# Optimization experiments

Measured on AMD Instinct MI355X. Metric: run time of the kernel, lower is better.

## Reference

```python
import jax, jax.numpy as jnp
import numpy as np
from jax import lax

M_BLOCKS = 4
D = 768
N = 8
L = 2040  # divisible by 1,2,3,4 so every block is full, matching the floor-based slicing


def setup_inputs() -> dict:
    key = jax.random.key(0)
    ks = jax.random.split(key, 7)
    X = jax.random.normal(ks[0], (N, L, D), dtype=jnp.float32)
    # char_mixer: Conv1d(d, d, kernel_size=3, padding='same')
    conv_w = jax.random.normal(ks[1], (D, D, 3), dtype=jnp.float32) * (1.0 / np.sqrt(3 * D))
    conv_b = jax.random.normal(ks[2], (D,), dtype=jnp.float32) * 0.01
    # F_R: Linear(d, 1)
    wr = jax.random.normal(ks[3], (D, 1), dtype=jnp.float32) * (1.0 / np.sqrt(D))
    br = jax.random.normal(ks[4], (1,), dtype=jnp.float32) * 0.01
    # F_D: Linear(d, d)
    wd = jax.random.normal(ks[5], (D, D), dtype=jnp.float32) * (1.0 / np.sqrt(D))
    bd = jax.random.normal(ks[6], (D,), dtype=jnp.float32) * 0.01
    return {"X": X, "conv_w": conv_w, "conv_b": conv_b, "wr": wr, "br": br, "wd": wd, "bd": bd}


def reference(X, conv_w, conv_b, wr, br, wd, bd):
    n, l, d = X.shape
    # char mixer: Conv1d over sequence (NCH layout)
    x = lax.conv_general_dilated(
        X.transpose(0, 2, 1), conv_w, window_strides=(1,), padding='SAME',
        dimension_numbers=('NCH', 'OIH', 'NCH'))
    x = (x + conv_b[None, :, None]).transpose(0, 2, 1)  # (N, L, d)

    # multi-scale block-pooled candidates X_B: (N, L, M, d)
    cands = []
    for b in range(1, M_BLOCKS + 1):  # small fixed loop over block sizes
        xb = x.reshape(n, l // b, b, d).mean(axis=2)       # mean-pool F over each block
        cands.append(jnp.repeat(xb, b, axis=1))            # broadcast block mean to positions
    XB = jnp.stack(cands, axis=2)

    # route scores F_R: Linear(d,1); softmax over trailing size-1 dim (faithful to source)
    P = jax.nn.softmax(XB @ wr + br, axis=-1)              # (N, L, M, 1)

    # calibration: softmax(P P^T) P
    P = P.reshape(n, l, M_BLOCKS)
    A = jax.nn.softmax(jnp.einsum('nlm,nkm->nlk', P, P), axis=-1)  # (N, L, L)
    P = jnp.einsum('nlk,nkm->nlm', A, P)                   # (N, L, M)

    # blend candidates and project with F_D
    X_hat = jnp.einsum('nlm,nlmd->nld', P, XB)             # (N, L, d)
    return X_hat @ wd + bd
```

## Files before the change

kernel.cpp:

```cpp
#include <hip/hip_runtime.h>

#define N_B    8
#define L_SEQ  2040
#define D_DIM  768
#define KDIM   2304
#define M_ROWS 16320
#define LPAD   2042

typedef __bf16 bf16x8 __attribute__((ext_vector_type(8)));
typedef float  f32x4  __attribute__((ext_vector_type(4)));

__device__ __forceinline__ unsigned short f2bf_u(float f) {
  union { float f; unsigned u; } v; v.f = f;
  unsigned u = v.u;
  return (unsigned short)((u + 0x7FFFu + ((u >> 16) & 1u)) >> 16);
}

__device__ __forceinline__ void async16(const unsigned short* g, const unsigned char* l) {
  __builtin_amdgcn_global_load_lds(
      (const __attribute__((address_space(1))) void*)g,
      (__attribute__((address_space(3))) void*)l, 16, 0, 0);
}

__global__ void k_pad(const float* __restrict__ X, unsigned short* __restrict__ Xpad) {
  size_t idx = ((size_t)blockIdx.x * 256 + threadIdx.x) * 4;
  const size_t per_n = (size_t)LPAD * D_DIM;
  int n = (int)(idx / per_n);
  size_t rem = idx - (size_t)n * per_n;
  int lp = (int)(rem / D_DIM);
  int d  = (int)(rem - (size_t)lp * D_DIM);
  ushort4 o;
  if (lp == 0 || lp == LPAD - 1) {
    o.x = 0; o.y = 0; o.z = 0; o.w = 0;
  } else {
    const float4 f = *(const float4*)&X[((size_t)n * L_SEQ + (lp - 1)) * D_DIM + d];
    o.x = f2bf_u(f.x); o.y = f2bf_u(f.y); o.z = f2bf_u(f.z); o.w = f2bf_u(f.w);
  }
  *(ushort4*)&Xpad[idx] = o;
}

__global__ void k_tr2(const float* __restrict__ wd, unsigned short* __restrict__ wdT,
                      const float* __restrict__ cw, unsigned short* __restrict__ cwT) {
  __shared__ float tile[32][33];
  const int z = blockIdx.z;
  const float* in = z ? cw : wd;
  unsigned short* out = z ? cwT : wdT;
  const int R = 768, C = z ? 2304 : 768;
  if (!z && blockIdx.x >= 24) return;
  int tx = threadIdx.x, ty = threadIdx.y;
  int c0 = blockIdx.x * 32;
  int r0 = blockIdx.y * 32;
  for (int i = ty; i < 32; i += 8) {
    int r = r0 + i, c = c0 + tx;
    tile[i][tx] = (r < R && c < C) ? in[(size_t)r * C + c] : 0.f;
  }
  __syncthreads();
  for (int i = ty; i < 32; i += 8) {
    int oc = c0 + i;
    int orr = r0 + tx;
    if (oc < C && orr < R) out[(size_t)oc * R + orr] = f2bf_u(tile[tx][i]);
  }
}

__global__ __launch_bounds__(256) void k_w2b(
    const unsigned short* __restrict__ wdT, const unsigned short* __restrict__ cwT,
    unsigned short* __restrict__ Bblk,
    const float* __restrict__ conv_b, const float* __restrict__ wd,
    const float* __restrict__ bd, float* __restrict__ bias2) {
  __shared__ unsigned short sA[128 * 32];
  __shared__ unsigned short sB[128 * 32];
  __shared__ float red[256];
  const int bid = blockIdx.x;
  const int t = threadIdx.x;

  if (bid >= 108) {
    const int b2 = bid - 108;
    const int o = b2 * 64 + (t & 63);
    const int sl = t >> 6;
    float acc = 0.f;
    for (int dm = sl * 192; dm < sl * 192 + 192; ++dm)
      acc += conv_b[dm] * wd[(size_t)dm * D_DIM + o];
    red[t] = acc;
    __syncthreads();
    if (t < 64)
      bias2[o] = 4.f * (red[t] + red[t + 64] + red[t + 128] + red[t + 192]) + bd[o];
    return;
  }

  const int bm = bid / 18, bn = bid - bm * 18;
  const int lane = t & 63, w = t >> 6;
  const int wr = w >> 1, wc = w & 1;
  const int lr = lane & 15, lg = lane >> 4;

  const int c0 = t, c1 = t + 256;
  const unsigned short* aB0 = wdT + (size_t)(bm * 128 + (c0 >> 2)) * 768 + (c0 & 3) * 8;
  const unsigned short* aB1 = wdT + (size_t)(bm * 128 + (c1 >> 2)) * 768 + (c1 & 3) * 8;
  const unsigned short* bB0 = cwT + (size_t)(bn * 128 + (c0 >> 2)) * 768 + (c0 & 3) * 8;
  const unsigned short* bB1 = cwT + (size_t)(bn * 128 + (c1 >> 2)) * 768 + (c1 & 3) * 8;

  f32x4 acc[4][4] = {};
  int aOff[4], bOff[4];
#pragma unroll
  for (int i = 0; i < 4; ++i) {
    aOff[i] = (wr * 64 + i * 16 + lr) * 4 + lg;
    bOff[i] = (wc * 64 + i * 16 + lr) * 4 + lg;
  }
  const bf16x8* At = (const bf16x8*)sA;
  const bf16x8* Bt = (const bf16x8*)sB;

  for (int kt = 0; kt < 24; ++kt) {
    const int ko = kt * 32;
    __syncthreads();
    async16(aB0 + ko, (const unsigned char*)&sA[c0 * 8]);
    async16(aB1 + ko, (const unsigned char*)&sA[c1 * 8]);
    async16(bB0 + ko, (const unsigned char*)&sB[c0 * 8]);
    async16(bB1 + ko, (const unsigned char*)&sB[c1 * 8]);
    __syncthreads();
    bf16x8 av[4], bv[4];
#pragma unroll
    for (int i = 0; i < 4; ++i) { av[i] = At[aOff[i]]; bv[i] = Bt[bOff[i]]; }
#pragma unroll
    for (int mi = 0; mi < 4; ++mi)
#pragma unroll
      for (int ni = 0; ni < 4; ++ni)
        acc[mi][ni] = __builtin_amdgcn_mfma_f32_16x16x32_bf16(av[mi], bv[ni], acc[mi][ni], 0, 0, 0);
  }

#pragma unroll
  for (int ni = 0; ni < 4; ++ni) {
    const int jp = bn * 128 + wc * 64 + ni * 16 + lr;
    const int di = jp / 3;
    const int kk = jp - di * 3;
    const int j = kk * 768 + di;
    const int kt2 = j >> 6, rem = j & 63;
    const int kh = rem >> 5, o = (rem >> 3) & 3, e = rem & 7;
    const size_t jbase = (size_t)kt2 * 16384 + kh * 8192 + o * 128 + e;
#pragma unroll
    for (int mi = 0; mi < 4; ++mi) {
      const int row0 = bm * 128 + wr * 64 + mi * 16 + lg * 4;
      f32x4 v = acc[mi][ni];
#pragma unroll
      for (int i = 0; i < 4; ++i) {
        const int dd = row0 + i;
        const int p = dd >> 8, cl = dd & 255, blk = cl >> 4, r = cl & 15;
        Bblk[(size_t)p * 589824 + jbase + blk * 512 + r * 8] = f2bf_u(v[i]);
      }
    }
  }
}

__global__ __launch_bounds__(512, 2) void k_conv192(
    const unsigned short* __restrict__ Xpad, const unsigned short* __restrict__ Bblk,
    const float* __restrict__ bias2, float* __restrict__ Y) {
  __shared__ unsigned char lds[114688];

  const int tid = threadIdx.x;
  const int lane = tid & 63;
  const int wid = tid >> 6;
  const int wr = wid >> 2, wc = wid & 3;

  const int bid = blockIdx.x;
  const int xcd = bid & 7, idx = bid >> 3;
  const int swz = (xcd < 7 ? xcd * 32 : 224 + (xcd - 7) * 31) + idx;
  const int bm = swz / 3, bn = swz - bm * 3;

  const unsigned short *aS0, *aS1, *aS2;
  {
#define ACHUNK(rr, dst) { \
    int c = tid + (rr) * 512; \
    int kh = c / 768, q = c - kh * 768; \
    int li = q & 63; \
    int rl = (q >> 6) * 16 + (li & 15); \
    int m = bm * 192 + rl; \
    int n = m / L_SEQ, l = m - n * L_SEQ; \
    dst = Xpad + (size_t)(n * LPAD + l) * D_DIM + kh * 32 + (li >> 4) * 8; }
    ACHUNK(0, aS0) ACHUNK(1, aS1) ACHUNK(2, aS2)
#undef ACHUNK
  }
  const unsigned short* bS = Bblk + (size_t)bn * 589824 + tid * 8;
  const int dA0 = tid * 16, dA1 = dA0 + 8192, dA2 = dA0 + 16384;
  const int dB0 = 24576 + tid * 16, dB1 = dB0 + 8192, dB2 = dB0 + 16384, dB3 = dB0 + 24576;

  const int aRd0 = wr * 6144 + lane * 16;
  const int bRd0 = 24576 + wc * 4096 + lane * 16;

  f32x4 acc[6][4] = {};
  bf16x8 av[6], bv[2];

#define STG(src, koff, dst) async16((src) + (koff), lds + nbb + (dst))
#define LD_AV(kh) \
    _Pragma("unroll") \
    for (int mi = 0; mi < 6; ++mi) \
      av[mi] = *(const bf16x8*)(lds + cb + aRd0 + (kh) * 12288 + mi * 1024);
#define LD_BV(kh, nh) \
    bv[0] = *(const bf16x8*)(lds + cb + bRd0 + (kh) * 16384 + (2 * (nh)) * 1024); \
    bv[1] = *(const bf16x8*)(lds + cb + bRd0 + (kh) * 16384 + (2 * (nh) + 1) * 1024);
#define MF12(nh) \
    __builtin_amdgcn_s_setprio(1); \
    _Pragma("unroll") \
    for (int mi = 0; mi < 6; ++mi) { \
      acc[mi][2 * (nh)]     = __builtin_amdgcn_mfma_f32_16x16x32_bf16(av[mi], bv[0], acc[mi][2 * (nh)], 0, 0, 0); \
      acc[mi][2 * (nh) + 1] = __builtin_amdgcn_mfma_f32_16x16x32_bf16(av[mi], bv[1], acc[mi][2 * (nh) + 1], 0, 0, 0); \
    } \
    __builtin_amdgcn_s_setprio(0);
#define BARR asm volatile("s_barrier" ::: "memory")
#define VM(n) asm volatile("s_waitcnt vmcnt(" #n ")" ::: "memory")
#define LGKM0 asm volatile("s_waitcnt lgkmcnt(0)" ::: "memory")

  {
    const int nbb = 0;
    STG(aS0, 0, dA0); STG(aS1, 0, dA1);
    STG(bS, 0, dB0);  STG(bS, 4096, dB1);
    STG(aS2, 0, dA2);
    STG(bS, 8192, dB2); STG(bS, 12288, dB3);
  }
  VM(3);
  BARR;

  for (int t = 0; t < 36; ++t) {
    const int cb = (t & 1) * 57344;
    const int nbb = ((t & 1) ^ 1) * 57344;
    const bool st = (t < 35);
    const int aoff = (t + 1) * 64;
    const size_t boff = (size_t)(t + 1) * 16384;
    LD_AV(0); LD_BV(0, 0);
    if (st) { STG(aS0, aoff, dA0); STG(aS1, aoff, dA1); }
    BARR;
    MF12(0);
    BARR;
    LD_BV(0, 1);
    if (st) { STG(bS, boff, dB0); STG(bS, boff + 4096, dB1); }
    BARR;
    MF12(1);
    if (st) { VM(4); } else { VM(0); }
    BARR;
    LD_AV(1); LD_BV(1, 0);
    if (st) { STG(aS2, aoff, dA2); STG(bS, boff + 8192, dB2); }
    BARR;
    MF12(0);
    BARR;
    LD_BV(1, 1);
    if (st) { STG(bS, boff + 12288, dB3); }
    BARR;
    MF12(1);
    VM(3);
    BARR;
  }

  const int lr = lane & 15, lg = lane >> 4;
  const f32x4 bias = *(const f32x4*)&bias2[bn * 256 + lane * 4];
#pragma unroll
  for (int p = 0; p < 2; ++p) {
    if (p) { BARR; }
    if (wr == p) {
#pragma unroll
      for (int mi = 0; mi < 6; ++mi)
#pragma unroll
        for (int ni = 0; ni < 4; ++ni)
#pragma unroll
          for (int i = 0; i < 4; ++i)
            *(float*)(lds + ((mi * 16 + lg * 4 + i) * 256 + (wc * 64 + ni * 16 + lr)) * 4) =
                acc[mi][ni][i];
    }
    LGKM0;
    BARR;
    f32x4 y[12];
#pragma unroll
    for (int i = 0; i < 12; ++i)
      y[i] = *(const f32x4*)(lds + ((wid * 12 + i) * 256 + lane * 4) * 4);
    f32x4 m2[6], m3[4], m4[3];
#pragma unroll
    for (int j = 0; j < 6; ++j) m2[j] = (y[2 * j] + y[2 * j + 1]) * 0.5f;
#pragma unroll
    for (int j = 0; j < 4; ++j) m3[j] = (y[3 * j] + y[3 * j + 1] + y[3 * j + 2]) * (1.f / 3.f);
#pragma unroll
    for (int j = 0; j < 3; ++j) m4[j] = (y[4 * j] + y[4 * j + 1] + y[4 * j + 2] + y[4 * j + 3]) * 0.25f;
    const int grow0 = bm * 192 + p * 96 + wid * 12;
#pragma unroll
    for (int i = 0; i < 12; ++i) {
      f32x4 o = y[i] + m2[i >> 1] + m3[i / 3] + m4[i >> 2] + bias;
      *(f32x4*)&Y[(size_t)(grow0 + i) * D_DIM + bn * 256 + lane * 4] = o;
    }
  }
#undef STG
#undef LD_AV
#undef LD_BV
#undef MF12
#undef BARR
#undef VM
#undef LGKM0
}

extern "C" void kernel_launch(void* const* d_in, const int* in_sizes, int n_in,
                              void* d_out, int out_size, void* d_ws, size_t ws_size,
                              hipStream_t stream) {
  const float* X      = (const float*)d_in[0];
  const float* conv_w = (const float*)d_in[1];
  const float* conv_b = (const float*)d_in[2];
  const float* wd     = (const float*)d_in[5];
  const float* bd     = (const float*)d_in[6];
  float* out = (float*)d_out;

  const size_t off_Xpad  = 0;
  const size_t off_wdT   = 25092096;
  const size_t off_cwT   = 26271744;
  const size_t off_Bblk  = 29810688;
  const size_t off_bias2 = 33349632;
  const size_t NEED      = 33352704;
  if (ws_size < NEED) return;

  char* ws = (char*)d_ws;
  unsigned short* Xpad  = (unsigned short*)(ws + off_Xpad);
  unsigned short* wdT   = (unsigned short*)(ws + off_wdT);
  unsigned short* cwT   = (unsigned short*)(ws + off_cwT);
  unsigned short* Bblk  = (unsigned short*)(ws + off_Bblk);
  float*          bias2 = (float*)(ws + off_bias2);

  k_pad<<<12252, 256, 0, stream>>>(X, Xpad);
  k_tr2<<<dim3(72, 24, 2), dim3(32, 8), 0, stream>>>(wd, wdT, conv_w, cwT);
  k_w2b<<<120, 256, 0, stream>>>(wdT, cwT, Bblk, conv_b, wd, bd, bias2);
  k_conv192<<<255, 512, 0, stream>>>(Xpad, Bblk, bias2, out);
}
```

Before: 98.48 us.

## Replace fine-grained barrier schedule with one sync per K-step in GEMM loop

The main GEMM loop used to interleave half-tile LDS reads, async global-to-LDS stages and MFMA groups, separated by many raw s_barrier and partial vmcnt waits. Now each half K-step loads all A and B fragments and issues 24 MFMAs at once, and there is a single __syncthreads at the end of each iteration. This cuts barrier count and simplifies the code. The cost is coarser overlap: __syncthreads waits for all outstanding loads, and the larger register footprint for B fragments may weaken latency hiding.

```diff
diff --git a/kernel.cpp b/kernel.cpp
--- a/kernel.cpp
+++ b/kernel.cpp
@@ -185,37 +185,32 @@
   const int bRd0 = 24576 + wc * 4096 + lane * 16;
 
   f32x4 acc[6][4] = {};
-  bf16x8 av[6], bv[2];
+  bf16x8 av[6], bv[4];
 
 #define STG(src, koff, dst) async16((src) + (koff), lds + nbb + (dst))
-#define LD_AV(kh) \
+#define LD_A(kh) \
     _Pragma("unroll") \
     for (int mi = 0; mi < 6; ++mi) \
       av[mi] = *(const bf16x8*)(lds + cb + aRd0 + (kh) * 12288 + mi * 1024);
-#define LD_BV(kh, nh) \
-    bv[0] = *(const bf16x8*)(lds + cb + bRd0 + (kh) * 16384 + (2 * (nh)) * 1024); \
-    bv[1] = *(const bf16x8*)(lds + cb + bRd0 + (kh) * 16384 + (2 * (nh) + 1) * 1024);
-#define MF12(nh) \
+#define LD_B(kh) \
+    _Pragma("unroll") \
+    for (int ni = 0; ni < 4; ++ni) \
+      bv[ni] = *(const bf16x8*)(lds + cb + bRd0 + (kh) * 16384 + (ni) * 1024);
+#define MF24 \
     __builtin_amdgcn_s_setprio(1); \
     _Pragma("unroll") \
-    for (int mi = 0; mi < 6; ++mi) { \
-      acc[mi][2 * (nh)]     = __builtin_amdgcn_mfma_f32_16x16x32_bf16(av[mi], bv[0], acc[mi][2 * (nh)], 0, 0, 0); \
-      acc[mi][2 * (nh) + 1] = __builtin_amdgcn_mfma_f32_16x16x32_bf16(av[mi], bv[1], acc[mi][2 * (nh) + 1], 0, 0, 0); \
-    } \
+    for (int mi = 0; mi < 6; ++mi) \
+      _Pragma("unroll") \
+      for (int ni = 0; ni < 4; ++ni) \
+        acc[mi][ni] = __builtin_amdgcn_mfma_f32_16x16x32_bf16(av[mi], bv[ni], acc[mi][ni], 0, 0, 0); \
     __builtin_amdgcn_s_setprio(0);
-#define BARR asm volatile("s_barrier" ::: "memory")
-#define VM(n) asm volatile("s_waitcnt vmcnt(" #n ")" ::: "memory")
-#define LGKM0 asm volatile("s_waitcnt lgkmcnt(0)" ::: "memory")
 
   {
     const int nbb = 0;
-    STG(aS0, 0, dA0); STG(aS1, 0, dA1);
-    STG(bS, 0, dB0);  STG(bS, 4096, dB1);
-    STG(aS2, 0, dA2);
-    STG(bS, 8192, dB2); STG(bS, 12288, dB3);
-  }
-  VM(3);
-  BARR;
+    STG(aS0, 0, dA0); STG(aS1, 0, dA1); STG(aS2, 0, dA2);
+    STG(bS, 0, dB0);  STG(bS, 4096, dB1); STG(bS, 8192, dB2); STG(bS, 12288, dB3);
+  }
+  __syncthreads();
 
   for (int t = 0; t < 36; ++t) {
     const int cb = (t & 1) * 57344;
@@ -223,35 +218,27 @@
     const bool st = (t < 35);
     const int aoff = (t + 1) * 64;
     const size_t boff = (size_t)(t + 1) * 16384;
-    LD_AV(0); LD_BV(0, 0);
-    if (st) { STG(aS0, aoff, dA0); STG(aS1, aoff, dA1); }
-    BARR;
-    MF12(0);
-    BARR;
-    LD_BV(0, 1);
-    if (st) { STG(bS, boff, dB0); STG(bS, boff + 4096, dB1); }
-    BARR;
-    MF12(1);
-    if (st) { VM(4); } else { VM(0); }
-    BARR;
-    LD_AV(1); LD_BV(1, 0);
-    if (st) { STG(aS2, aoff, dA2); STG(bS, boff + 8192, dB2); }
-    BARR;
-    MF12(0);
-    BARR;
-    LD_BV(1, 1);
-    if (st) { STG(bS, boff + 12288, dB3); }
-    BARR;
-    MF12(1);
-    VM(3);
-    BARR;
+
+    LD_A(0); LD_B(0);
+    if (st) {
+      STG(aS0, aoff, dA0); STG(aS1, aoff, dA1);
+      STG(bS, boff, dB0);  STG(bS, boff + 4096, dB1);
+    }
+    MF24;
+    LD_A(1); LD_B(1);
+    if (st) {
+      STG(aS2, aoff, dA2);
+      STG(bS, boff + 8192, dB2); STG(bS, boff + 12288, dB3);
+    }
+    MF24;
+    __syncthreads();
   }
 
   const int lr = lane & 15, lg = lane >> 4;
   const f32x4 bias = *(const f32x4*)&bias2[bn * 256 + lane * 4];
 #pragma unroll
   for (int p = 0; p < 2; ++p) {
-    if (p) { BARR; }
+    if (p) __syncthreads();
     if (wr == p) {
 #pragma unroll
       for (int mi = 0; mi < 6; ++mi)
@@ -262,8 +249,7 @@
             *(float*)(lds + ((mi * 16 + lg * 4 + i) * 256 + (wc * 64 + ni * 16 + lr)) * 4) =
                 acc[mi][ni][i];
     }
-    LGKM0;
-    BARR;
+    __syncthreads();
     f32x4 y[12];
 #pragma unroll
     for (int i = 0; i < 12; ++i)
@@ -283,12 +269,9 @@
     }
   }
 #undef STG
-#undef LD_AV
-#undef LD_BV
-#undef MF12
-#undef BARR
-#undef VM
-#undef LGKM0
+#undef LD_A
+#undef LD_B
+#undef MF24
 }
 
 extern "C" void kernel_launch(void* const* d_in, const int* in_sizes, int n_in,
```

Measured after the change: 102.0 us. +3.6%, slower.
